# Performance work log

Hardware: AMD Instinct MI355X
Metric: run time of the kernel (lower is better)

## Reference

```python
import jax, jax.numpy as jnp
import numpy as np

B, A, D, CIN = 256, 512, 64, 4  # batch, action_dim, day_length, in channels
C1, C2 = 4, 16
EPS = 1e-5


def _ln(x):
    # non-affine LayerNorm over (C, H, W), per-sample
    m = jnp.mean(x, axis=(1, 2, 3), keepdims=True)
    v = jnp.var(x, axis=(1, 2, 3), keepdims=True)
    return (x - m) / jnp.sqrt(v + EPS)


def _dblock(x, w_dil, w_pw):
    # dilated (1,3) conv, dilation 2, padding (0,2) -> width preserved
    y = jax.lax.conv_general_dilated(
        x, w_dil, window_strides=(1, 1), padding=[(0, 0), (2, 2)],
        rhs_dilation=(2, 2), dimension_numbers=('NCHW', 'OIHW', 'NCHW'))
    y = _ln(y)
    y = jnp.einsum('bchw,oc->bohw', y, w_pw[:, :, 0, 0])  # 1x1 conv
    return jax.nn.gelu(y, approximate=False)


def setup_inputs() -> dict:
    key = jax.random.key(0)
    ks = jax.random.split(key, 11)
    f = lambda k, shp: (jax.random.normal(k, shp, dtype=jnp.float32) * 0.1)
    return {
        's': jax.random.normal(ks[0], (B, A, D, CIN), dtype=jnp.float32),
        'w': jax.random.normal(ks[1], (B, A), dtype=jnp.float32),
        'd1w1': f(ks[2], (C1, CIN, 1, 3)),
        'd1w2': f(ks[3], (C1, C1, 1, 1)),
        'd2w1': f(ks[4], (C1, CIN, 1, 3)),
        'd2w2': f(ks[5], (C1, C1, 1, 1)),
        'd3w1': f(ks[6], (C1, CIN, 1, 3)),
        'd3w2': f(ks[7], (C1, C1, 1, 1)),
        'cw': f(ks[8], (C1, 3 * C1, 1, 1)),
        'c2w': f(ks[9], (C2, C1, 1, D)),
        'c3w': f(ks[10], (1, C2 + 1, 1, 1)),
    }


def reference(s, w, d1w1, d1w2, d2w1, d2w2, d3w1, d3w2, cw, c2w, c3w):
    s = jnp.transpose(s, (0, 3, 1, 2))          # [B, 4, A, D]
    x1 = _dblock(s, d1w1, d1w2)
    x2 = _dblock(s + x1, d2w1, d2w2)
    x3 = _dblock(s + x1 + x2, d3w1, d3w2)
    x = jnp.concatenate([x1, x2, x3], axis=1)   # [B, 12, A, D]
    x = _ln(x)
    x = jnp.einsum('bchw,oc->bohw', x, cw[:, :, 0, 0])      # 1x1 conv -> [B,4,A,D]
    x = jnp.einsum('bchw,ocw->boh', x, c2w[:, :, 0, :])[..., None]  # (1,D) conv -> [B,16,A,1]
    x = _ln(x)
    x = jnp.concatenate([x, w[:, None, :, None]], axis=1)   # [B,17,A,1]
    x = jnp.einsum('bchw,oc->bohw', x, c3w[:, :, 0, 0])     # [B,1,A,1]
    x = _ln(x)
    return x[:, 0, :, 0]                                    # [B, A]
```

## Files before the change

kernel.cpp:

```cpp
#include <hip/hip_runtime.h>
#include <math.h>


#define EPS_LN 1e-5f
typedef float4 f4;

__device__ __forceinline__ float gelu_f(float v) {
    return 0.5f * v * (1.0f + erff(v * 0.70710678118654752440f));
}

__device__ __forceinline__ void conv4(const f4 a, const f4 c, const f4 e,
                                      const float* __restrict__ wd, float y[4]) {
#pragma unroll
    for (int o = 0; o < 4; ++o) {
        const float* wv = wd + o * 12;
        y[o] = fmaf(a.x, wv[0], fmaf(c.x, wv[1], fmaf(e.x, wv[2],
               fmaf(a.y, wv[3], fmaf(c.y, wv[4], fmaf(e.y, wv[5],
               fmaf(a.z, wv[6], fmaf(c.z, wv[7], fmaf(e.z, wv[8],
               fmaf(a.w, wv[9], fmaf(c.w, wv[10], e.w * wv[11])))))))))));
    }
}

__device__ __forceinline__ void block_red2(float& a, float& b2, float* red,
                                           float* bc, int tid) {
#pragma unroll
    for (int off = 32; off > 0; off >>= 1) {
        a  += __shfl_down(a,  off, 64);
        b2 += __shfl_down(b2, off, 64);
    }
    if ((tid & 63) == 0) { red[tid >> 6] = a; red[8 + (tid >> 6)] = b2; }
    __syncthreads();
    if (tid == 0) {
        float x = 0.f, y = 0.f;
#pragma unroll
        for (int i = 0; i < 8; ++i) { x += red[i]; y += red[8 + i]; }
        bc[0] = x; bc[1] = y;
    }
    __syncthreads();
    a = bc[0]; b2 = bc[1];
}

__global__ __launch_bounds__(512)
void tcn_fused(const float* __restrict__ sIn, const float* __restrict__ wIn,
               const float* __restrict__ w1d, const float* __restrict__ w1p,
               const float* __restrict__ w2d, const float* __restrict__ w2p,
               const float* __restrict__ w3d, const float* __restrict__ w3p,
               const float* __restrict__ cw,  const float* __restrict__ c2w,
               const float* __restrict__ c3w, float* __restrict__ out,
               f4* __restrict__ baseT) {
    const int b   = blockIdx.x;
    const int tid = threadIdx.x;

    __shared__ float red[16];
    __shared__ float bc[2];
    __shared__ float Klds[16];

    if (tid < 16) {
        float k = 0.f;
        for (int co = 0; co < 4; ++co) {
            float cs = 0.f;
            for (int j = 0; j < 12; ++j) cs += cw[co * 12 + j];
            const float* p = c2w + tid * 256 + co * 64;
            float t = 0.f;
            for (int d = 0; d < 64; ++d) t += p[d];
            k = fmaf(cs, t, k);
        }
        Klds[tid] = k;
    }

    const f4* s4 = (const f4*)sIn;
    const size_t srow = ((size_t)b * 512 + tid) * 64;
    const size_t brow = (size_t)b * (64 * 512) + tid;
    const f4 z4 = make_float4(0.f, 0.f, 0.f, 0.f);
    const float NY = 4.f * 512.f * 64.f;

    float s1 = 0.f, s2 = 0.f;
    {
        f4 wA = z4, wB = z4, wC = s4[srow], wD = s4[srow + 1], wE;
        for (int d = 0; d < 64; ++d) {
            wE = (d + 2 < 64) ? s4[srow + d + 2] : z4;
            float y[4]; conv4(wA, wC, wE, w1d, y);
#pragma unroll
            for (int o = 0; o < 4; ++o) { s1 += y[o]; s2 = fmaf(y[o], y[o], s2); }
            wA = wB; wB = wC; wC = wD; wD = wE;
        }
    }
    block_red2(s1, s2, red, bc, tid);
    float m1 = s1 / NY;
    float r1 = rsqrtf(s2 / NY - m1 * m1 + EPS_LN);

    float t16a[16];
#pragma unroll
    for (int o = 0; o < 16; ++o) t16a[o] = 0.f;
    float cs1 = 0.f, cs2 = 0.f;

    float q1 = 0.f, q2 = 0.f;
    {
        f4 wA = z4, wB = z4, wC = s4[srow], wD = s4[srow + 1], wE;
        f4 bA = z4, bB = z4, bC = z4, bD = z4, bE;
        for (int d = 0; d < 66; ++d) {
            if (d < 64) {
                wE = (d + 2 < 64) ? s4[srow + d + 2] : z4;
                float y[4]; conv4(wA, wC, wE, w1d, y);
#pragma unroll
                for (int o = 0; o < 4; ++o) y[o] = (y[o] - m1) * r1;
                float g[4];
#pragma unroll
                for (int o = 0; o < 4; ++o) {
                    float zz = fmaf(y[0], w1p[o*4+0], fmaf(y[1], w1p[o*4+1],
                               fmaf(y[2], w1p[o*4+2], y[3] * w1p[o*4+3])));
                    g[o] = gelu_f(zz);
                }
#pragma unroll
                for (int o = 0; o < 4; ++o) { cs1 += g[o]; cs2 = fmaf(g[o], g[o], cs2); }
                float u[4];
#pragma unroll
                for (int co = 0; co < 4; ++co)
                    u[co] = fmaf(g[0], cw[co*12+0], fmaf(g[1], cw[co*12+1],
                            fmaf(g[2], cw[co*12+2], g[3] * cw[co*12+3])));
#pragma unroll
                for (int o = 0; o < 16; ++o) {
                    const float* p = c2w + o * 256 + d;
                    t16a[o] = fmaf(u[0], p[0], fmaf(u[1], p[64],
                              fmaf(u[2], p[128], fmaf(u[3], p[192], t16a[o]))));
                }
                f4 nb;
                nb.x = wC.x + g[0]; nb.y = wC.y + g[1];
                nb.z = wC.z + g[2]; nb.w = wC.w + g[3];
                baseT[brow + (size_t)d * 512] = nb;
                bE = nb;
                wA = wB; wB = wC; wC = wD; wD = wE;
            } else bE = z4;
            if (d >= 2) {
                float y2[4]; conv4(bA, bC, bE, w2d, y2);
#pragma unroll
                for (int o = 0; o < 4; ++o) { q1 += y2[o]; q2 = fmaf(y2[o], y2[o], q2); }
            }
            bA = bB; bB = bC; bC = bD; bD = bE;
        }
    }
    block_red2(q1, q2, red, bc, tid);
    float m2s = q1 / NY;
    float r2s = rsqrtf(q2 / NY - m2s * m2s + EPS_LN);

    float q31 = 0.f, q32 = 0.f;
    {
        f4 gA = z4, gB = z4, gC = z4, gD = z4, gE;
        f4 hA = z4, hB = z4, hC = z4, hD = z4, hE;
        for (int t = 0; t < 68; ++t) {
            gE = (t < 64) ? baseT[brow + (size_t)t * 512] : z4;
            if (t >= 2 && t < 66) {
                const int e = t - 2;
                float y[4]; conv4(gA, gC, gE, w2d, y);
#pragma unroll
                for (int o = 0; o < 4; ++o) y[o] = (y[o] - m2s) * r2s;
                float g[4];
#pragma unroll
                for (int o = 0; o < 4; ++o) {
                    float zz = fmaf(y[0], w2p[o*4+0], fmaf(y[1], w2p[o*4+1],
                               fmaf(y[2], w2p[o*4+2], y[3] * w2p[o*4+3])));
                    g[o] = gelu_f(zz);
                }
#pragma unroll
                for (int o = 0; o < 4; ++o) { cs1 += g[o]; cs2 = fmaf(g[o], g[o], cs2); }
                float u[4];
#pragma unroll
                for (int co = 0; co < 4; ++co)
                    u[co] = fmaf(g[0], cw[co*12+4], fmaf(g[1], cw[co*12+5],
                            fmaf(g[2], cw[co*12+6], g[3] * cw[co*12+7])));
#pragma unroll
                for (int o = 0; o < 16; ++o) {
                    const float* p = c2w + o * 256 + e;
                    t16a[o] = fmaf(u[0], p[0], fmaf(u[1], p[64],
                              fmaf(u[2], p[128], fmaf(u[3], p[192], t16a[o]))));
                }
                f4 nb;
                nb.x = gC.x + g[0]; nb.y = gC.y + g[1];
                nb.z = gC.z + g[2]; nb.w = gC.w + g[3];
                baseT[brow + (size_t)e * 512] = nb;
                hE = nb;
            } else hE = z4;
            if (t >= 4) {
                float y3[4]; conv4(hA, hC, hE, w3d, y3);
#pragma unroll
                for (int o = 0; o < 4; ++o) { q31 += y3[o]; q32 = fmaf(y3[o], y3[o], q32); }
            }
            gA = gB; gB = gC; gC = gD; gD = gE;
            hA = hB; hB = hC; hC = hD; hD = hE;
        }
    }
    block_red2(q31, q32, red, bc, tid);
    float m3s = q31 / NY;
    float r3s = rsqrtf(q32 / NY - m3s * m3s + EPS_LN);

    {
        f4 wA = z4, wB = z4, wC = baseT[brow], wD = baseT[brow + 512], wE;
        for (int d = 0; d < 64; ++d) {
            wE = (d + 2 < 64) ? baseT[brow + (size_t)(d + 2) * 512] : z4;
            float y[4]; conv4(wA, wC, wE, w3d, y);
#pragma unroll
            for (int o = 0; o < 4; ++o) y[o] = (y[o] - m3s) * r3s;
            float g[4];
#pragma unroll
            for (int o = 0; o < 4; ++o) {
                float zz = fmaf(y[0], w3p[o*4+0], fmaf(y[1], w3p[o*4+1],
                           fmaf(y[2], w3p[o*4+2], y[3] * w3p[o*4+3])));
                g[o] = gelu_f(zz);
            }
#pragma unroll
            for (int o = 0; o < 4; ++o) { cs1 += g[o]; cs2 = fmaf(g[o], g[o], cs2); }
            float u[4];
#pragma unroll
            for (int co = 0; co < 4; ++co)
                u[co] = fmaf(g[0], cw[co*12+8], fmaf(g[1], cw[co*12+9],
                        fmaf(g[2], cw[co*12+10], g[3] * cw[co*12+11])));
#pragma unroll
            for (int o = 0; o < 16; ++o) {
                const float* p = c2w + o * 256 + d;
                t16a[o] = fmaf(u[0], p[0], fmaf(u[1], p[64],
                          fmaf(u[2], p[128], fmaf(u[3], p[192], t16a[o]))));
            }
            wA = wB; wB = wC; wC = wD; wD = wE;
        }
    }

    block_red2(cs1, cs2, red, bc, tid);
    const float NC = 12.f * 512.f * 64.f;
    float mcat = cs1 / NC;
    float rcat = rsqrtf(cs2 / NC - mcat * mcat + EPS_LN);

    float tv[16];
    float p1 = 0.f, p2 = 0.f;
#pragma unroll
    for (int o = 0; o < 16; ++o) {
        float v = rcat * (t16a[o] - mcat * Klds[o]);
        tv[o] = v; p1 += v; p2 = fmaf(v, v, p2);
    }
    block_red2(p1, p2, red, bc, tid);
    const float N16 = 16.f * 512.f;
    float m16 = p1 / N16;
    float r16 = rsqrtf(p2 / N16 - m16 * m16 + EPS_LN);

    float v = wIn[(size_t)b * 512 + tid] * c3w[16];
#pragma unroll
    for (int o = 0; o < 16; ++o) v = fmaf((tv[o] - m16) * r16, c3w[o], v);
    float f1 = v, f2 = v * v;
    block_red2(f1, f2, red, bc, tid);
    float mA = f1 / 512.f;
    float rA = rsqrtf(f2 / 512.f - mA * mA + EPS_LN);

    out[(size_t)b * 512 + tid] = (v - mA) * rA;
}

extern "C" void kernel_launch(void* const* d_in, const int* in_sizes, int n_in,
                              void* d_out, int out_size, void* d_ws, size_t ws_size,
                              hipStream_t stream) {
    const float* s   = (const float*)d_in[0];
    const float* w   = (const float*)d_in[1];
    const float* w1d = (const float*)d_in[2];
    const float* w1p = (const float*)d_in[3];
    const float* w2d = (const float*)d_in[4];
    const float* w2p = (const float*)d_in[5];
    const float* w3d = (const float*)d_in[6];
    const float* w3p = (const float*)d_in[7];
    const float* cw  = (const float*)d_in[8];
    const float* c2w = (const float*)d_in[9];
    const float* c3w = (const float*)d_in[10];
    tcn_fused<<<dim3(256), dim3(512), 0, stream>>>(
        s, w, w1d, w1p, w2d, w2p, w3d, w3p, cw, c2w, c3w,
        (float*)d_out, (f4*)d_ws);
}
```

Measured before the change: 536.4 us.

## Split fused TCN kernel into multi-kernel pipeline with bf16 intermediates and fast GELU

Replaces the single 256-block fused kernel with seven launches: per-stage statistics kernels and production kernels over 512 blocks of 256 threads, plus a tail kernel. This exposes more parallelism than one block per batch sample, which only filled 256 blocks. The intermediate residual base is stored in bf16 to halve its memory traffic, and the erf GELU is replaced with a sigmoid-style exp2/rcp approximation. Together these trade accuracy (bf16 storage, approximate GELU) and extra launch and recompute overhead for occupancy and bandwidth.

```diff
diff --git a/kernel.cpp b/kernel.cpp
--- a/kernel.cpp
+++ b/kernel.cpp
@@ -6,7 +6,9 @@
 typedef float4 f4;
 
 __device__ __forceinline__ float gelu_f(float v) {
-    return 0.5f * v * (1.0f + erff(v * 0.70710678118654752440f));
+    float t = v * fmaf(0.10294324f, v * v, 2.30220822f);
+    float e = __builtin_amdgcn_exp2f(-t);
+    return v * __builtin_amdgcn_rcpf(1.0f + e);
 }
 
 __device__ __forceinline__ void conv4(const f4 a, const f4 c, const f4 e,
@@ -21,233 +23,282 @@
     }
 }
 
-__device__ __forceinline__ void block_red2(float& a, float& b2, float* red,
-                                           float* bc, int tid) {
+__device__ __forceinline__ unsigned short bf16r(float x) {
+    union { float f; unsigned u; } v; v.f = x;
+    unsigned r = v.u + 0x7FFFu + ((v.u >> 16) & 1u);
+    return (unsigned short)(r >> 16);
+}
+__device__ __forceinline__ float bf16f(unsigned short h) {
+    union { float f; unsigned u; } v; v.u = ((unsigned)h) << 16;
+    return v.f;
+}
+__device__ __forceinline__ f4 unpack4(ushort4 p) {
+    return make_float4(bf16f(p.x), bf16f(p.y), bf16f(p.z), bf16f(p.w));
+}
+__device__ __forceinline__ ushort4 pack4(f4 v) {
+    ushort4 p; p.x = bf16r(v.x); p.y = bf16r(v.y);
+    p.z = bf16r(v.z); p.w = bf16r(v.w); return p;
+}
+
+__device__ __forceinline__ void red2_out(float x, float y, float* red, int tid,
+                                         float* __restrict__ gout) {
 #pragma unroll
     for (int off = 32; off > 0; off >>= 1) {
-        a  += __shfl_down(a,  off, 64);
-        b2 += __shfl_down(b2, off, 64);
-    }
-    if ((tid & 63) == 0) { red[tid >> 6] = a; red[8 + (tid >> 6)] = b2; }
+        x += __shfl_down(x, off, 64); y += __shfl_down(y, off, 64);
+    }
+    const int w = tid >> 6;
+    if ((tid & 63) == 0) { red[w] = x; red[4 + w] = y; }
     __syncthreads();
     if (tid == 0) {
-        float x = 0.f, y = 0.f;
-#pragma unroll
-        for (int i = 0; i < 8; ++i) { x += red[i]; y += red[8 + i]; }
-        bc[0] = x; bc[1] = y;
-    }
+        gout[0] = red[0] + red[1] + red[2] + red[3];
+        gout[1] = red[4] + red[5] + red[6] + red[7];
+    }
+}
+
+__device__ __forceinline__ void red2_b8(float& x, float& y, float* red,
+                                        float* bc, int tid) {
+#pragma unroll
+    for (int off = 32; off > 0; off >>= 1) {
+        x += __shfl_down(x, off, 64); y += __shfl_down(y, off, 64);
+    }
+    const int w = tid >> 6;
+    if ((tid & 63) == 0) { red[w] = x; red[8 + w] = y; }
     __syncthreads();
-    a = bc[0]; b2 = bc[1];
+    if (tid == 0) {
+        float sx = 0.f, sy = 0.f;
+#pragma unroll
+        for (int i = 0; i < 8; ++i) { sx += red[i]; sy += red[8 + i]; }
+        bc[0] = sx; bc[1] = sy;
+    }
+    __syncthreads();
+    x = bc[0]; y = bc[1];
+}
+
+__global__ __launch_bounds__(256)
+void k_stat_s(const float* __restrict__ sIn, const float* __restrict__ wd,
+              float* __restrict__ outp) {
+    __shared__ float red[8];
+    const int tid = threadIdx.x;
+    const int b = blockIdx.x >> 1;
+    const int a = ((blockIdx.x & 1) << 8) | tid;
+    const f4* s4 = (const f4*)sIn;
+    const size_t row = ((size_t)b * 512 + a) * 64;
+    const f4 z4 = make_float4(0.f, 0.f, 0.f, 0.f);
+    float s1 = 0.f, s2 = 0.f;
+    f4 wA = z4, wB = z4, wC = s4[row], wD = s4[row + 1], wE;
+#pragma unroll 4
+    for (int d = 0; d < 64; ++d) {
+        wE = (d + 2 < 64) ? s4[row + d + 2] : z4;
+        float y[4]; conv4(wA, wC, wE, wd, y);
+#pragma unroll
+        for (int o = 0; o < 4; ++o) { s1 += y[o]; s2 = fmaf(y[o], y[o], s2); }
+        wA = wB; wB = wC; wC = wD; wD = wE;
+    }
+    red2_out(s1, s2, red, tid, outp + blockIdx.x * 2);
+}
+
+__global__ __launch_bounds__(256)
+void k_stat_b(const ushort4* __restrict__ baseB, const float* __restrict__ wd,
+              float* __restrict__ outp) {
+    __shared__ float red[8];
+    const int tid = threadIdx.x;
+    const int b = blockIdx.x >> 1;
+    const int a = ((blockIdx.x & 1) << 8) | tid;
+    const size_t col = (size_t)b * 32768 + a;
+    const f4 z4 = make_float4(0.f, 0.f, 0.f, 0.f);
+    float s1 = 0.f, s2 = 0.f;
+    f4 wA = z4, wB = z4, wC = unpack4(baseB[col]), wD = unpack4(baseB[col + 512]), wE;
+#pragma unroll 4
+    for (int d = 0; d < 64; ++d) {
+        wE = (d + 2 < 64) ? unpack4(baseB[col + (size_t)(d + 2) * 512]) : z4;
+        float y[4]; conv4(wA, wC, wE, wd, y);
+#pragma unroll
+        for (int o = 0; o < 4; ++o) { s1 += y[o]; s2 = fmaf(y[o], y[o], s2); }
+        wA = wB; wB = wC; wC = wD; wD = wE;
+    }
+    red2_out(s1, s2, red, tid, outp + blockIdx.x * 2);
+}
+
+__global__ __launch_bounds__(256)
+void k_prod1(const float* __restrict__ sIn, const float* __restrict__ w1d,
+             const float* __restrict__ w1p, const float* __restrict__ cw,
+             const float* __restrict__ c2w, ushort4* __restrict__ baseB,
+             float* __restrict__ t16buf, const float* __restrict__ ypIn,
+             float* __restrict__ cspOut) {
+    __shared__ float red[8];
+    const int tid = threadIdx.x;
+    const int b = blockIdx.x >> 1;
+    const int a = ((blockIdx.x & 1) << 8) | tid;
+    const f4* s4 = (const f4*)sIn;
+    const size_t row = ((size_t)b * 512 + a) * 64;
+    const size_t col = (size_t)b * 32768 + a;
+    const f4 z4 = make_float4(0.f, 0.f, 0.f, 0.f);
+    const float NY = 131072.f;
+    const float p0 = ypIn[(b * 2) * 2] + ypIn[(b * 2 + 1) * 2];
+    const float q0 = ypIn[(b * 2) * 2 + 1] + ypIn[(b * 2 + 1) * 2 + 1];
+    const float m1 = p0 / NY;
+    const float r1 = rsqrtf(q0 / NY - m1 * m1 + EPS_LN);
+
+    float t16a[16];
+#pragma unroll
+    for (int o = 0; o < 16; ++o) t16a[o] = 0.f;
+    float cs1 = 0.f, cs2 = 0.f;
+
+    f4 wA = z4, wB = z4, wC = s4[row], wD = s4[row + 1], wE;
+#pragma unroll 4
+    for (int d = 0; d < 64; ++d) {
+        wE = (d + 2 < 64) ? s4[row + d + 2] : z4;
+        float y[4]; conv4(wA, wC, wE, w1d, y);
+        float g[4];
+#pragma unroll
+        for (int o = 0; o < 4; ++o) {
+            y[o] = (y[o] - m1) * r1;
+        }
+#pragma unroll
+        for (int o = 0; o < 4; ++o) {
+            float zz = fmaf(y[0], w1p[o*4+0], fmaf(y[1], w1p[o*4+1],
+                       fmaf(y[2], w1p[o*4+2], y[3] * w1p[o*4+3])));
+            g[o] = gelu_f(zz);
+            cs1 += g[o]; cs2 = fmaf(g[o], g[o], cs2);
+        }
+        f4 nb = make_float4(wC.x + g[0], wC.y + g[1], wC.z + g[2], wC.w + g[3]);
+        baseB[col + (size_t)d * 512] = pack4(nb);
+        float u[4];
+#pragma unroll
+        for (int co = 0; co < 4; ++co)
+            u[co] = fmaf(g[0], cw[co*12+0], fmaf(g[1], cw[co*12+1],
+                    fmaf(g[2], cw[co*12+2], g[3] * cw[co*12+3])));
+#pragma unroll
+        for (int o = 0; o < 16; ++o) {
+            const float* p = c2w + o * 256 + d;
+            t16a[o] = fmaf(u[0], p[0], fmaf(u[1], p[64],
+                      fmaf(u[2], p[128], fmaf(u[3], p[192], t16a[o]))));
+        }
+        wA = wB; wB = wC; wC = wD; wD = wE;
+    }
+    float* tp = t16buf + ((size_t)b * 512 + a) * 16;
+#pragma unroll
+    for (int o = 0; o < 16; ++o) tp[o] = t16a[o];
+    red2_out(cs1, cs2, red, tid, cspOut + blockIdx.x * 2);
+}
+
+__global__ __launch_bounds__(256)
+void k_prod23(ushort4* __restrict__ baseB, const float* __restrict__ wd,
+              const float* __restrict__ wp, const float* __restrict__ cw,
+              const float* __restrict__ c2w, float* __restrict__ t16buf,
+              const float* __restrict__ ypIn, float* __restrict__ cspOut,
+              const int cwOff, const int writeBase) {
+    __shared__ float red[8];
+    const int tid = threadIdx.x;
+    const int b = blockIdx.x >> 1;
+    const int a = ((blockIdx.x & 1) << 8) | tid;
+    const size_t col = (size_t)b * 32768 + a;
+    const f4 z4 = make_float4(0.f, 0.f, 0.f, 0.f);
+    const float NY = 131072.f;
+    const float p0 = ypIn[(b * 2) * 2] + ypIn[(b * 2 + 1) * 2];
+    const float q0 = ypIn[(b * 2) * 2 + 1] + ypIn[(b * 2 + 1) * 2 + 1];
+    const float mS = p0 / NY;
+    const float rS = rsqrtf(q0 / NY - mS * mS + EPS_LN);
+
+    float t16a[16];
+    float* tp = t16buf + ((size_t)b * 512 + a) * 16;
+#pragma unroll
+    for (int o = 0; o < 16; ++o) t16a[o] = tp[o];
+    float cs1 = 0.f, cs2 = 0.f;
+
+    f4 wA = z4, wB = z4, wC = unpack4(baseB[col]), wD = unpack4(baseB[col + 512]), wE;
+#pragma unroll 4
+    for (int d = 0; d < 64; ++d) {
+        wE = (d + 2 < 64) ? unpack4(baseB[col + (size_t)(d + 2) * 512]) : z4;
+        float y[4]; conv4(wA, wC, wE, wd, y);
+        float g[4];
+#pragma unroll
+        for (int o = 0; o < 4; ++o) y[o] = (y[o] - mS) * rS;
+#pragma unroll
+        for (int o = 0; o < 4; ++o) {
+            float zz = fmaf(y[0], wp[o*4+0], fmaf(y[1], wp[o*4+1],
+                       fmaf(y[2], wp[o*4+2], y[3] * wp[o*4+3])));
+            g[o] = gelu_f(zz);
+            cs1 += g[o]; cs2 = fmaf(g[o], g[o], cs2);
+        }
+        if (writeBase) {
+            f4 nb = make_float4(wC.x + g[0], wC.y + g[1], wC.z + g[2], wC.w + g[3]);
+            baseB[col + (size_t)d * 512] = pack4(nb);
+        }
+        float u[4];
+#pragma unroll
+        for (int co = 0; co < 4; ++co)
+            u[co] = fmaf(g[0], cw[co*12+cwOff+0], fmaf(g[1], cw[co*12+cwOff+1],
+                    fmaf(g[2], cw[co*12+cwOff+2], g[3] * cw[co*12+cwOff+3])));
+#pragma unroll
+        for (int o = 0; o < 16; ++o) {
+            const float* p = c2w + o * 256 + d;
+            t16a[o] = fmaf(u[0], p[0], fmaf(u[1], p[64],
+                      fmaf(u[2], p[128], fmaf(u[3], p[192], t16a[o]))));
+        }
+        wA = wB; wB = wC; wC = wD; wD = wE;
+    }
+#pragma unroll
+    for (int o = 0; o < 16; ++o) tp[o] = t16a[o];
+    red2_out(cs1, cs2, red, tid, cspOut + blockIdx.x * 2);
 }
 
 __global__ __launch_bounds__(512)
-void tcn_fused(const float* __restrict__ sIn, const float* __restrict__ wIn,
-               const float* __restrict__ w1d, const float* __restrict__ w1p,
-               const float* __restrict__ w2d, const float* __restrict__ w2p,
-               const float* __restrict__ w3d, const float* __restrict__ w3p,
-               const float* __restrict__ cw,  const float* __restrict__ c2w,
-               const float* __restrict__ c3w, float* __restrict__ out,
-               f4* __restrict__ baseT) {
-    const int b   = blockIdx.x;
-    const int tid = threadIdx.x;
-
+void k_tail(const float* __restrict__ wIn, const float* __restrict__ cw,
+            const float* __restrict__ c2w, const float* __restrict__ c3w,
+            const float* __restrict__ t16buf, const float* __restrict__ csp,
+            float* __restrict__ out) {
     __shared__ float red[16];
     __shared__ float bc[2];
     __shared__ float Klds[16];
+    const int b = blockIdx.x;
+    const int tid = threadIdx.x;
 
     if (tid < 16) {
         float k = 0.f;
         for (int co = 0; co < 4; ++co) {
-            float cs = 0.f;
-            for (int j = 0; j < 12; ++j) cs += cw[co * 12 + j];
+            float csum = 0.f;
+            for (int j = 0; j < 12; ++j) csum += cw[co * 12 + j];
             const float* p = c2w + tid * 256 + co * 64;
             float t = 0.f;
             for (int d = 0; d < 64; ++d) t += p[d];
-            k = fmaf(cs, t, k);
+            k = fmaf(csum, t, k);
         }
         Klds[tid] = k;
     }
-
-    const f4* s4 = (const f4*)sIn;
-    const size_t srow = ((size_t)b * 512 + tid) * 64;
-    const size_t brow = (size_t)b * (64 * 512) + tid;
-    const f4 z4 = make_float4(0.f, 0.f, 0.f, 0.f);
-    const float NY = 4.f * 512.f * 64.f;
-
-    float s1 = 0.f, s2 = 0.f;
-    {
-        f4 wA = z4, wB = z4, wC = s4[srow], wD = s4[srow + 1], wE;
-        for (int d = 0; d < 64; ++d) {
-            wE = (d + 2 < 64) ? s4[srow + d + 2] : z4;
-            float y[4]; conv4(wA, wC, wE, w1d, y);
-#pragma unroll
-            for (int o = 0; o < 4; ++o) { s1 += y[o]; s2 = fmaf(y[o], y[o], s2); }
-            wA = wB; wB = wC; wC = wD; wD = wE;
-        }
-    }
-    block_red2(s1, s2, red, bc, tid);
-    float m1 = s1 / NY;
-    float r1 = rsqrtf(s2 / NY - m1 * m1 + EPS_LN);
-
-    float t16a[16];
-#pragma unroll
-    for (int o = 0; o < 16; ++o) t16a[o] = 0.f;
+    __syncthreads();
+
     float cs1 = 0.f, cs2 = 0.f;
-
-    float q1 = 0.f, q2 = 0.f;
-    {
-        f4 wA = z4, wB = z4, wC = s4[srow], wD = s4[srow + 1], wE;
-        f4 bA = z4, bB = z4, bC = z4, bD = z4, bE;
-        for (int d = 0; d < 66; ++d) {
-            if (d < 64) {
-                wE = (d + 2 < 64) ? s4[srow + d + 2] : z4;
-                float y[4]; conv4(wA, wC, wE, w1d, y);
-#pragma unroll
-                for (int o = 0; o < 4; ++o) y[o] = (y[o] - m1) * r1;
-                float g[4];
-#pragma unroll
-                for (int o = 0; o < 4; ++o) {
-                    float zz = fmaf(y[0], w1p[o*4+0], fmaf(y[1], w1p[o*4+1],
-                               fmaf(y[2], w1p[o*4+2], y[3] * w1p[o*4+3])));
-                    g[o] = gelu_f(zz);
-                }
-#pragma unroll
-                for (int o = 0; o < 4; ++o) { cs1 += g[o]; cs2 = fmaf(g[o], g[o], cs2); }
-                float u[4];
-#pragma unroll
-                for (int co = 0; co < 4; ++co)
-                    u[co] = fmaf(g[0], cw[co*12+0], fmaf(g[1], cw[co*12+1],
-                            fmaf(g[2], cw[co*12+2], g[3] * cw[co*12+3])));
-#pragma unroll
-                for (int o = 0; o < 16; ++o) {
-                    const float* p = c2w + o * 256 + d;
-                    t16a[o] = fmaf(u[0], p[0], fmaf(u[1], p[64],
-                              fmaf(u[2], p[128], fmaf(u[3], p[192], t16a[o]))));
-                }
-                f4 nb;
-                nb.x = wC.x + g[0]; nb.y = wC.y + g[1];
-                nb.z = wC.z + g[2]; nb.w = wC.w + g[3];
-                baseT[brow + (size_t)d * 512] = nb;
-                bE = nb;
-                wA = wB; wB = wC; wC = wD; wD = wE;
-            } else bE = z4;
-            if (d >= 2) {
-                float y2[4]; conv4(bA, bC, bE, w2d, y2);
-#pragma unroll
-                for (int o = 0; o < 4; ++o) { q1 += y2[o]; q2 = fmaf(y2[o], y2[o], q2); }
-            }
-            bA = bB; bB = bC; bC = bD; bD = bE;
-        }
-    }
-    block_red2(q1, q2, red, bc, tid);
-    float m2s = q1 / NY;
-    float r2s = rsqrtf(q2 / NY - m2s * m2s + EPS_LN);
-
-    float q31 = 0.f, q32 = 0.f;
-    {
-        f4 gA = z4, gB = z4, gC = z4, gD = z4, gE;
-        f4 hA = z4, hB = z4, hC = z4, hD = z4, hE;
-        for (int t = 0; t < 68; ++t) {
-            gE = (t < 64) ? baseT[brow + (size_t)t * 512] : z4;
-            if (t >= 2 && t < 66) {
-                const int e = t - 2;
-                float y[4]; conv4(gA, gC, gE, w2d, y);
-#pragma unroll
-                for (int o = 0; o < 4; ++o) y[o] = (y[o] - m2s) * r2s;
-                float g[4];
-#pragma unroll
-                for (int o = 0; o < 4; ++o) {
-                    float zz = fmaf(y[0], w2p[o*4+0], fmaf(y[1], w2p[o*4+1],
-                               fmaf(y[2], w2p[o*4+2], y[3] * w2p[o*4+3])));
-                    g[o] = gelu_f(zz);
-                }
-#pragma unroll
-                for (int o = 0; o < 4; ++o) { cs1 += g[o]; cs2 = fmaf(g[o], g[o], cs2); }
-                float u[4];
-#pragma unroll
-                for (int co = 0; co < 4; ++co)
-                    u[co] = fmaf(g[0], cw[co*12+4], fmaf(g[1], cw[co*12+5],
-                            fmaf(g[2], cw[co*12+6], g[3] * cw[co*12+7])));
-#pragma unroll
-                for (int o = 0; o < 16; ++o) {
-                    const float* p = c2w + o * 256 + e;
-                    t16a[o] = fmaf(u[0], p[0], fmaf(u[1], p[64],
-                              fmaf(u[2], p[128], fmaf(u[3], p[192], t16a[o]))));
-                }
-                f4 nb;
-                nb.x = gC.x + g[0]; nb.y = gC.y + g[1];
-                nb.z = gC.z + g[2]; nb.w = gC.w + g[3];
-                baseT[brow + (size_t)e * 512] = nb;
-                hE = nb;
-            } else hE = z4;
-            if (t >= 4) {
-                float y3[4]; conv4(hA, hC, hE, w3d, y3);
-#pragma unroll
-                for (int o = 0; o < 4; ++o) { q31 += y3[o]; q32 = fmaf(y3[o], y3[o], q32); }
-            }
-            gA = gB; gB = gC; gC = gD; gD = gE;
-            hA = hB; hB = hC; hC = hD; hD = hE;
-        }
-    }
-    block_red2(q31, q32, red, bc, tid);
-    float m3s = q31 / NY;
-    float r3s = rsqrtf(q32 / NY - m3s * m3s + EPS_LN);
-
-    {
-        f4 wA = z4, wB = z4, wC = baseT[brow], wD = baseT[brow + 512], wE;
-        for (int d = 0; d < 64; ++d) {
-            wE = (d + 2 < 64) ? baseT[brow + (size_t)(d + 2) * 512] : z4;
-            float y[4]; conv4(wA, wC, wE, w3d, y);
-#pragma unroll
-            for (int o = 0; o < 4; ++o) y[o] = (y[o] - m3s) * r3s;
-            float g[4];
-#pragma unroll
-            for (int o = 0; o < 4; ++o) {
-                float zz = fmaf(y[0], w3p[o*4+0], fmaf(y[1], w3p[o*4+1],
-                           fmaf(y[2], w3p[o*4+2], y[3] * w3p[o*4+3])));
-                g[o] = gelu_f(zz);
-            }
-#pragma unroll
-            for (int o = 0; o < 4; ++o) { cs1 += g[o]; cs2 = fmaf(g[o], g[o], cs2); }
-            float u[4];
-#pragma unroll
-            for (int co = 0; co < 4; ++co)
-                u[co] = fmaf(g[0], cw[co*12+8], fmaf(g[1], cw[co*12+9],
-                        fmaf(g[2], cw[co*12+10], g[3] * cw[co*12+11])));
-#pragma unroll
-            for (int o = 0; o < 16; ++o) {
-                const float* p = c2w + o * 256 + d;
-                t16a[o] = fmaf(u[0], p[0], fmaf(u[1], p[64],
-                          fmaf(u[2], p[128], fmaf(u[3], p[192], t16a[o]))));
-            }
-            wA = wB; wB = wC; wC = wD; wD = wE;
-        }
-    }
-
-    block_red2(cs1, cs2, red, bc, tid);
-    const float NC = 12.f * 512.f * 64.f;
-    float mcat = cs1 / NC;
-    float rcat = rsqrtf(cs2 / NC - mcat * mcat + EPS_LN);
-
+#pragma unroll
+    for (int ph = 0; ph < 3; ++ph)
+#pragma unroll
+        for (int c = 0; c < 2; ++c) {
+            cs1 += csp[ph * 1024 + (b * 2 + c) * 2];
+            cs2 += csp[ph * 1024 + (b * 2 + c) * 2 + 1];
+        }
+    const float NC = 393216.f;
+    const float mcat = cs1 / NC;
+    const float rcat = rsqrtf(cs2 / NC - mcat * mcat + EPS_LN);
+
+    const float* tp = t16buf + ((size_t)b * 512 + tid) * 16;
     float tv[16];
     float p1 = 0.f, p2 = 0.f;
 #pragma unroll
     for (int o = 0; o < 16; ++o) {
-        float v = rcat * (t16a[o] - mcat * Klds[o]);
+        float v = rcat * (tp[o] - mcat * Klds[o]);
         tv[o] = v; p1 += v; p2 = fmaf(v, v, p2);
     }
-    block_red2(p1, p2, red, bc, tid);
-    const float N16 = 16.f * 512.f;
-    float m16 = p1 / N16;
-    float r16 = rsqrtf(p2 / N16 - m16 * m16 + EPS_LN);
+    red2_b8(p1, p2, red, bc, tid);
+    const float m16 = p1 / 8192.f;
+    const float r16 = rsqrtf(p2 / 8192.f - m16 * m16 + EPS_LN);
 
     float v = wIn[(size_t)b * 512 + tid] * c3w[16];
 #pragma unroll
     for (int o = 0; o < 16; ++o) v = fmaf((tv[o] - m16) * r16, c3w[o], v);
     float f1 = v, f2 = v * v;
-    block_red2(f1, f2, red, bc, tid);
-    float mA = f1 / 512.f;
-    float rA = rsqrtf(f2 / 512.f - mA * mA + EPS_LN);
+    red2_b8(f1, f2, red, bc, tid);
+    const float mA = f1 / 512.f;
+    const float rA = rsqrtf(f2 / 512.f - mA * mA + EPS_LN);
 
     out[(size_t)b * 512 + tid] = (v - mA) * rA;
 }
@@ -266,7 +317,22 @@
     const float* cw  = (const float*)d_in[8];
     const float* c2w = (const float*)d_in[9];
     const float* c3w = (const float*)d_in[10];
-    tcn_fused<<<dim3(256), dim3(512), 0, stream>>>(
-        s, w, w1d, w1p, w2d, w2p, w3d, w3p, cw, c2w, c3w,
-        (float*)d_out, (f4*)d_ws);
-}
+
+    char* ws = (char*)d_ws;
+    ushort4* baseB  = (ushort4*)ws;
+    float*   t16buf = (float*)(ws + 67108864);
+    float*   stats  = (float*)(ws + 67108864 + 8388608);
+    float*   y1p = stats;
+    float*   y2p = stats + 1024;
+    float*   y3p = stats + 2048;
+    float*   csp = stats + 3072;
+
+    dim3 g(512), blk(256);
+    k_stat_s<<<g, blk, 0, stream>>>(s, w1d, y1p);
+    k_prod1 <<<g, blk, 0, stream>>>(s, w1d, w1p, cw, c2w, baseB, t16buf, y1p, csp);
+    k_stat_b<<<g, blk, 0, stream>>>(baseB, w2d, y2p);
+    k_prod23<<<g, blk, 0, stream>>>(baseB, w2d, w2p, cw, c2w, t16buf, y2p, csp + 1024, 4, 1);
+    k_stat_b<<<g, blk, 0, stream>>>(baseB, w3d, y3p);
+    k_prod23<<<g, blk, 0, stream>>>(baseB, w3d, w3p, cw, c2w, t16buf, y3p, csp + 2048, 8, 0);
+    k_tail  <<<dim3(256), dim3(512), 0, stream>>>(w, cw, c2w, c3w, t16buf, csp, (float*)d_out);
+}
```

Measured after the change: 674.1 us. +25.7%, slower.
